# Kernel tuning notes

Hardware: AMD Instinct MI355X
Metric: run time of the kernel (lower is better)

The kernel has to match this reference:

```python
import jax, jax.numpy as jnp
import numpy as np

N_NODES = 20000
N_EDGES = 320000
H = 128
IN = 256  # num_hidden + num_in
SCALE = 30.0
EPS = 1e-5


def _ln(x, g, b):
    m = jnp.mean(x, axis=-1, keepdims=True)
    v = jnp.var(x, axis=-1, keepdims=True)
    return (x - m) * jax.lax.rsqrt(v + EPS) * g + b


def setup_inputs() -> dict:
    key = jax.random.key(0)
    ks = jax.random.split(key, 16)
    s_in = 1.0 / np.sqrt(IN)
    s_h = 1.0 / np.sqrt(H)
    s_4h = 1.0 / np.sqrt(4 * H)
    return {
        "h_V": jax.random.normal(ks[0], (N_NODES, H), jnp.float32),
        "h_E": jax.random.normal(ks[1], (N_EDGES, IN), jnp.float32),
        "edge_idx": jax.random.randint(ks[2], (2, N_EDGES), 0, N_NODES, jnp.int32),
        # weights stored (in, out): y = x @ W + b (equivalent to torch Linear)
        "W1_w": jax.random.uniform(ks[3], (IN, H), jnp.float32, -s_in, s_in),
        "W1_b": jax.random.uniform(ks[4], (H,), jnp.float32, -s_in, s_in),
        "W2_w": jax.random.uniform(ks[5], (H, H), jnp.float32, -s_h, s_h),
        "W2_b": jax.random.uniform(ks[6], (H,), jnp.float32, -s_h, s_h),
        "W3_w": jax.random.uniform(ks[7], (H, H), jnp.float32, -s_h, s_h),
        "W3_b": jax.random.uniform(ks[8], (H,), jnp.float32, -s_h, s_h),
        "n1_g": jnp.ones((H,), jnp.float32),
        "n1_b": jnp.zeros((H,), jnp.float32),
        "d1_w": jax.random.uniform(ks[9], (H, 4 * H), jnp.float32, -s_h, s_h),
        "d1_b": jax.random.uniform(ks[10], (4 * H,), jnp.float32, -s_h, s_h),
        "d2_w": jax.random.uniform(ks[11], (4 * H, H), jnp.float32, -s_4h, s_4h),
        "d2_b": jax.random.uniform(ks[12], (H,), jnp.float32, -s_4h, s_4h),
        "n2_g": jnp.ones((H,), jnp.float32),
        "n2_b": jnp.zeros((H,), jnp.float32),
    }


def reference(h_V, h_E, edge_idx, W1_w, W1_b, W2_w, W2_b, W3_w, W3_b,
              n1_g, n1_b, d1_w, d1_b, d2_w, d2_b, n2_g, n2_b):
    gelu = lambda x: jax.nn.gelu(x, approximate=False)  # torch F.gelu default = erf
    src_idx = edge_idx[0]
    # edge MLP: W3(gelu(W2(gelu(W1(h_E)))))
    h_message = gelu(h_E @ W1_w + W1_b)
    h_message = gelu(h_message @ W2_w + W2_b)
    h_message = h_message @ W3_w + W3_b
    # scatter_sum over source node, then scale
    dh = jax.ops.segment_sum(h_message, src_idx, num_segments=N_NODES) / SCALE
    h_V = _ln(h_V + dh, n1_g, n1_b)  # dropout is identity at eval
    dh = gelu(h_V @ d1_w + d1_b) @ d2_w + d2_b
    h_V = _ln(h_V + dh, n2_g, n2_b)
    return h_V
```

## Files before the change

### kernel.cpp

```cpp
#include <hip/hip_runtime.h>
#include <hip/hip_bf16.h>
#include <math.h>

#define NNODES 20000
#define NEDGES 320000
#define HDIM   128
#define INDIM  256
#define INV_SCALE (1.0f/30.0f)
#define LN_EPS 1e-5f

typedef __bf16 bf16x8 __attribute__((ext_vector_type(8)));
typedef float  f32x4  __attribute__((ext_vector_type(4)));
typedef _Float16 half4_t __attribute__((ext_vector_type(4)));
typedef _Float16 half8_t __attribute__((ext_vector_type(8)));
typedef unsigned short ushort_t;

__device__ __forceinline__ unsigned short f2bf(float f) {
    union { __hip_bfloat16 h; unsigned short u; } c;
    c.h = __float2bfloat16(f);
    return c.u;
}

__device__ __forceinline__ float gelu_fast(float x) {
    const float z = x * (1.595769122f + 0.071354816f * x * x);
    return x / (1.0f + __expf(-z));
}

__device__ __forceinline__ f32x4 mfma_bf16(bf16x8 a, bf16x8 b, f32x4 c) {
    return __builtin_amdgcn_mfma_f32_16x16x32_bf16(a, b, c, 0, 0, 0);
}

#define CVT8(dst, v0, v1) { union { bf16x8 v; ushort_t u[8]; } c_; \
    c_.u[0] = f2bf((v0).x); c_.u[1] = f2bf((v0).y); c_.u[2] = f2bf((v0).z); c_.u[3] = f2bf((v0).w); \
    c_.u[4] = f2bf((v1).x); c_.u[5] = f2bf((v1).y); c_.u[6] = f2bf((v1).z); c_.u[7] = f2bf((v1).w); \
    (dst) = c_.v; }

__global__ void prep_all(const float* __restrict__ W1, const float* __restrict__ W2,
                         const float* __restrict__ W3, ushort_t* __restrict__ WswE,
                         const float* __restrict__ D1, const float* __restrict__ D2,
                         ushort_t* __restrict__ D1sw, ushort_t* __restrict__ D2sw,
                         const int* __restrict__ src, int* __restrict__ cnt) {
    const int id = blockIdx.x * 256 + threadIdx.x;
    if (id < 65536) {
        const float* W; int base, idx; bool perm = false;
        if (id < 32768)      { W = W1; base = 0;     idx = id; }
        else if (id < 49152) { W = W2; base = 32768; idx = id - 32768; }
        else                 { W = W3; base = 49152; idx = id - 49152; perm = true; }
        const int j = idx & 7, lane = (idx >> 3) & 63, t = (idx >> 9) & 7, s = idx >> 12;
        const int k = s * 32 + (lane >> 4) * 8 + j;
        const int n = perm ? (2 * ((t >> 1) * 16 + (lane & 15)) + (t & 1))
                           : (t * 16 + (lane & 15));
        WswE[base + idx] = f2bf(W[k * HDIM + n]);
    } else if (id < 196608) {
        if (!D1sw) return;
        const int nid = id - 65536;
        if (nid < 65536) {
            const int idx = nid;
            const int j = idx & 7, lane = (idx >> 3) & 63, f = idx >> 9;
            const int t = f & 31, s = f >> 5;
            const int k = s * 32 + (lane >> 4) * 8 + j;
            const int n = t * 16 + (lane & 15);
            D1sw[idx] = f2bf(D1[k * 512 + n]);
        } else {
            const int idx = nid - 65536;
            const int j = idx & 7, lane = (idx >> 3) & 63, f = idx >> 9;
            const int t = f & 7, s = f >> 3;
            const int k = s * 32 + (lane >> 4) * 8 + j;
            const int n = t * 16 + (lane & 15);
            D2sw[idx] = f2bf(D2[k * HDIM + n]);
        }
    } else {
        if (!cnt) return;
        const int e = id - 196608;
        if (e < NEDGES) atomicAdd(&cnt[src[e]], 1);
    }
}

__launch_bounds__(1024)
__global__ void scan_counts(const int* __restrict__ cnt,
                            int* __restrict__ off, int* __restrict__ off2) {
    __shared__ int tot[1024];
    const int t = threadIdx.x;
    const int base = t * 20;
    int local[20]; int s = 0;
    #pragma unroll
    for (int i = 0; i < 20; ++i) {
        const int v = (base + i < NNODES) ? cnt[base + i] : 0;
        local[i] = s; s += v;
    }
    tot[t] = s;
    __syncthreads();
    for (int d = 1; d < 1024; d <<= 1) {
        const int v = (t >= d) ? tot[t - d] : 0;
        __syncthreads();
        tot[t] += v;
        __syncthreads();
    }
    const int excl = (t == 0) ? 0 : tot[t - 1];
    #pragma unroll
    for (int i = 0; i < 20; ++i)
        if (base + i < NNODES) { off[base + i] = excl + local[i]; off2[base + i] = excl + local[i]; }
    if (t == 1023) off[NNODES] = NEDGES;
}

__global__ void fill_perm(const int* __restrict__ src, int* __restrict__ off2,
                          int* __restrict__ perm) {
    const int e = blockIdx.x * 256 + threadIdx.x;
    if (e < NEDGES) {
        const int p = atomicAdd(&off2[src[e]], 1);
        perm[p] = e;
    }
}

#define A1H 136
#define SY  136

__launch_bounds__(256, 4)
__global__ void edge_mlp_v3(const float* __restrict__ hE,
                            const ushort_t* __restrict__ Wsw,
                            const float* __restrict__ b1,
                            const float* __restrict__ b2,
                            const float* __restrict__ b3,
                            _Float16* __restrict__ msg) {
    __shared__ __align__(16) ushort_t A1h[64 * A1H];
    __shared__ __align__(16) ushort_t A2[64 * SY];

    const int tid = threadIdx.x;
    const int wave = tid >> 6, lane = tid & 63;
    const int quad = lane >> 4, l16 = lane & 15;
    const size_t e0 = (size_t)blockIdx.x * 64;
    const int T0 = wave * 2;

    const int srow = tid >> 2, sq = tid & 3;
    const float4* sp = (const float4*)(hE + (e0 + srow) * INDIM) + sq * 8;
    ushort_t* sd = A1h + srow * A1H + sq * 32;

    float4 rg[8];
    #pragma unroll
    for (int i = 0; i < 8; ++i) rg[i] = sp[i];
    #pragma unroll
    for (int i = 0; i < 4; ++i) {
        bf16x8 v; CVT8(v, rg[2 * i], rg[2 * i + 1]);
        *(bf16x8*)(sd + i * 8) = v;
    }
    #pragma unroll
    for (int i = 0; i < 8; ++i) rg[i] = sp[32 + i];

    f32x4 acc[4][2];
    bf16x8 bcur[2], bnxt[2];

    #pragma unroll
    for (int t = 0; t < 2; ++t) {
        const float bv = b1[(T0 + t) * 16 + l16];
        #pragma unroll
        for (int rt = 0; rt < 4; ++rt) acc[rt][t] = (f32x4){bv, bv, bv, bv};
    }
    bcur[0] = *(const bf16x8*)(Wsw + (size_t)((T0 + 0) * 64 + lane) * 8);
    bcur[1] = *(const bf16x8*)(Wsw + (size_t)((T0 + 1) * 64 + lane) * 8);
    __syncthreads();

    #pragma unroll
    for (int s = 0; s < 4; ++s) {
        bnxt[0] = *(const bf16x8*)(Wsw + (size_t)(((s + 1) * 8 + T0 + 0) * 64 + lane) * 8);
        bnxt[1] = *(const bf16x8*)(Wsw + (size_t)(((s + 1) * 8 + T0 + 1) * 64 + lane) * 8);
        bf16x8 a[4];
        #pragma unroll
        for (int rt = 0; rt < 4; ++rt)
            a[rt] = *(const bf16x8*)(A1h + (rt * 16 + l16) * A1H + s * 32 + quad * 8);
        #pragma unroll
        for (int rt = 0; rt < 4; ++rt) {
            acc[rt][0] = mfma_bf16(a[rt], bcur[0], acc[rt][0]);
            acc[rt][1] = mfma_bf16(a[rt], bcur[1], acc[rt][1]);
        }
        bcur[0] = bnxt[0]; bcur[1] = bnxt[1];
    }
    __syncthreads();

    #pragma unroll
    for (int i = 0; i < 4; ++i) {
        bf16x8 v; CVT8(v, rg[2 * i], rg[2 * i + 1]);
        *(bf16x8*)(sd + i * 8) = v;
    }
    __syncthreads();

    #pragma unroll
    for (int s = 4; s < 8; ++s) {
        if (s < 7) {
            bnxt[0] = *(const bf16x8*)(Wsw + (size_t)(((s + 1) * 8 + T0 + 0) * 64 + lane) * 8);
            bnxt[1] = *(const bf16x8*)(Wsw + (size_t)(((s + 1) * 8 + T0 + 1) * 64 + lane) * 8);
        }
        bf16x8 a[4];
        #pragma unroll
        for (int rt = 0; rt < 4; ++rt)
            a[rt] = *(const bf16x8*)(A1h + (rt * 16 + l16) * A1H + (s - 4) * 32 + quad * 8);
        #pragma unroll
        for (int rt = 0; rt < 4; ++rt) {
            acc[rt][0] = mfma_bf16(a[rt], bcur[0], acc[rt][0]);
            acc[rt][1] = mfma_bf16(a[rt], bcur[1], acc[rt][1]);
        }
        bcur[0] = bnxt[0]; bcur[1] = bnxt[1];
    }
    #pragma unroll
    for (int rt = 0; rt < 4; ++rt)
        #pragma unroll
        for (int t = 0; t < 2; ++t)
            #pragma unroll
            for (int r = 0; r < 4; ++r)
                A2[(rt * 16 + quad * 4 + r) * SY + (T0 + t) * 16 + l16] =
                    f2bf(gelu_fast(acc[rt][t][r]));
    __syncthreads();

    #pragma unroll
    for (int t = 0; t < 2; ++t) {
        const float bv = b2[(T0 + t) * 16 + l16];
        #pragma unroll
        for (int rt = 0; rt < 4; ++rt) acc[rt][t] = (f32x4){bv, bv, bv, bv};
    }
    bcur[0] = *(const bf16x8*)(Wsw + 32768 + (size_t)((T0 + 0) * 64 + lane) * 8);
    bcur[1] = *(const bf16x8*)(Wsw + 32768 + (size_t)((T0 + 1) * 64 + lane) * 8);
    #pragma unroll
    for (int s = 0; s < 4; ++s) {
        if (s < 3) {
            bnxt[0] = *(const bf16x8*)(Wsw + 32768 + (size_t)(((s + 1) * 8 + T0 + 0) * 64 + lane) * 8);
            bnxt[1] = *(const bf16x8*)(Wsw + 32768 + (size_t)(((s + 1) * 8 + T0 + 1) * 64 + lane) * 8);
        }
        bf16x8 a[4];
        #pragma unroll
        for (int rt = 0; rt < 4; ++rt)
            a[rt] = *(const bf16x8*)(A2 + (rt * 16 + l16) * SY + s * 32 + quad * 8);
        #pragma unroll
        for (int rt = 0; rt < 4; ++rt) {
            acc[rt][0] = mfma_bf16(a[rt], bcur[0], acc[rt][0]);
            acc[rt][1] = mfma_bf16(a[rt], bcur[1], acc[rt][1]);
        }
        bcur[0] = bnxt[0]; bcur[1] = bnxt[1];
    }
    __syncthreads();
    #pragma unroll
    for (int rt = 0; rt < 4; ++rt)
        #pragma unroll
        for (int t = 0; t < 2; ++t)
            #pragma unroll
            for (int r = 0; r < 4; ++r)
                A2[(rt * 16 + quad * 4 + r) * SY + (T0 + t) * 16 + l16] =
                    f2bf(gelu_fast(acc[rt][t][r]));
    __syncthreads();

    #pragma unroll
    for (int t = 0; t < 2; ++t) {
        const float bv = b3[2 * (wave * 16 + l16) + t];
        #pragma unroll
        for (int rt = 0; rt < 4; ++rt) acc[rt][t] = (f32x4){bv, bv, bv, bv};
    }
    bcur[0] = *(const bf16x8*)(Wsw + 49152 + (size_t)((T0 + 0) * 64 + lane) * 8);
    bcur[1] = *(const bf16x8*)(Wsw + 49152 + (size_t)((T0 + 1) * 64 + lane) * 8);
    #pragma unroll
    for (int s = 0; s < 4; ++s) {
        if (s < 3) {
            bnxt[0] = *(const bf16x8*)(Wsw + 49152 + (size_t)(((s + 1) * 8 + T0 + 0) * 64 + lane) * 8);
            bnxt[1] = *(const bf16x8*)(Wsw + 49152 + (size_t)(((s + 1) * 8 + T0 + 1) * 64 + lane) * 8);
        }
        bf16x8 a[4];
        #pragma unroll
        for (int rt = 0; rt < 4; ++rt)
            a[rt] = *(const bf16x8*)(A2 + (rt * 16 + l16) * SY + s * 32 + quad * 8);
        #pragma unroll
        for (int rt = 0; rt < 4; ++rt) {
            acc[rt][0] = mfma_bf16(a[rt], bcur[0], acc[rt][0]);
            acc[rt][1] = mfma_bf16(a[rt], bcur[1], acc[rt][1]);
        }
        bcur[0] = bnxt[0]; bcur[1] = bnxt[1];
    }

    #pragma unroll
    for (int rt = 0; rt < 4; ++rt)
        #pragma unroll
        for (int r = 0; r < 4; ++r) {
            const size_t row = e0 + rt * 16 + quad * 4 + r;
            union { _Float16 h[2]; unsigned int u; } pk;
            pk.h[0] = (_Float16)acc[rt][0][r];
            pk.h[1] = (_Float16)acc[rt][1][r];
            ((unsigned int*)(msg + row * HDIM))[wave * 16 + l16] = pk.u;
        }
}

__launch_bounds__(256)
__global__ void gather_sum(const _Float16* __restrict__ msg,
                           const int* __restrict__ perm,
                           const int* __restrict__ off,
                           const float* __restrict__ hV,
                           float* __restrict__ xout) {
    const int tid = threadIdx.x;
    const int slot = tid >> 5, l32 = tid & 31;
    const int node = blockIdx.x * 8 + slot;
    const int j0 = off[node], j1 = off[node + 1];
    float a0 = 0.f, a1 = 0.f, a2 = 0.f, a3 = 0.f;
    int j = j0;
    for (; j + 1 < j1; j += 2) {
        const int ea = perm[j], eb = perm[j + 1];
        const half4_t ma = *(const half4_t*)(msg + (size_t)ea * HDIM + l32 * 4);
        const half4_t mb = *(const half4_t*)(msg + (size_t)eb * HDIM + l32 * 4);
        a0 += (float)ma[0] + (float)mb[0];
        a1 += (float)ma[1] + (float)mb[1];
        a2 += (float)ma[2] + (float)mb[2];
        a3 += (float)ma[3] + (float)mb[3];
    }
    if (j < j1) {
        const int ea = perm[j];
        const half4_t ma = *(const half4_t*)(msg + (size_t)ea * HDIM + l32 * 4);
        a0 += (float)ma[0]; a1 += (float)ma[1]; a2 += (float)ma[2]; a3 += (float)ma[3];
    }
    const float4 hv = *(const float4*)(hV + (size_t)node * HDIM + l32 * 4);
    const float4 o = {hv.x + a0 * INV_SCALE, hv.y + a1 * INV_SCALE,
                      hv.z + a2 * INV_SCALE, hv.w + a3 * INV_SCALE};
    *(float4*)(xout + (size_t)node * HDIM + l32 * 4) = o;
}

__launch_bounds__(256)
__global__ void node_mfma_x(const float* __restrict__ xin,
                            const float* __restrict__ n1g, const float* __restrict__ n1b,
                            const ushort_t* __restrict__ D1sw, const float* __restrict__ D1b,
                            const ushort_t* __restrict__ D2sw, const float* __restrict__ D2b,
                            const float* __restrict__ n2g, const float* __restrict__ n2b,
                            float* __restrict__ out) {
    __shared__ __align__(16) float xs[32 * HDIM];
    __shared__ __align__(16) ushort_t h1a[32 * SY];
    __shared__ __align__(16) ushort_t ua[32 * 520];
    __shared__ float mu_s[32], rs_s[32];

    const int tid = threadIdx.x;
    const int wave = tid >> 6, lane = tid & 63;
    const int quad = lane >> 4, l16 = lane & 15;
    const int n0 = blockIdx.x * 32;

    #pragma unroll
    for (int it = 0; it < 4; ++it) {
        const int f4 = it * 256 + tid;
        ((float4*)xs)[f4] = ((const float4*)(xin + (size_t)n0 * HDIM))[f4];
    }
    __syncthreads();

    {
        const int row = tid >> 3, q = tid & 7;
        float s = 0.f, s2 = 0.f;
        #pragma unroll
        for (int c = 0; c < 16; ++c) { const float v = xs[row * HDIM + q * 16 + c]; s += v; s2 += v * v; }
        #pragma unroll
        for (int o = 1; o < 8; o <<= 1) { s += __shfl_xor(s, o); s2 += __shfl_xor(s2, o); }
        if (q == 0) {
            const float m = s * (1.0f / HDIM);
            mu_s[row] = m;
            rs_s[row] = rsqrtf(s2 * (1.0f / HDIM) - m * m + LN_EPS);
        }
    }
    __syncthreads();

    #pragma unroll
    for (int it = 0; it < 2; ++it) {
        const int g = it * 256 + tid;
        const int row = g >> 4, col = (g & 15) * 8;
        const float mu = mu_s[row], rs = rs_s[row];
        union { bf16x8 v; ushort_t u[8]; } c;
        #pragma unroll
        for (int jj = 0; jj < 8; ++jj) {
            const float h1 = (xs[row * HDIM + col + jj] - mu) * rs * n1g[col + jj] + n1b[col + jj];
            c.u[jj] = f2bf(h1);
        }
        *(bf16x8*)(h1a + row * SY + col) = c.v;
    }
    __syncthreads();

    {
        f32x4 acc1[2][8];
        #pragma unroll
        for (int t = 0; t < 8; ++t) {
            const float bv = D1b[wave * 128 + t * 16 + l16];
            acc1[0][t] = (f32x4){bv, bv, bv, bv};
            acc1[1][t] = acc1[0][t];
        }
        #pragma unroll
        for (int s = 0; s < 4; ++s) {
            bf16x8 a[2];
            #pragma unroll
            for (int rt = 0; rt < 2; ++rt)
                a[rt] = *(const bf16x8*)(h1a + (rt * 16 + l16) * SY + s * 32 + quad * 8);
            #pragma unroll
            for (int t = 0; t < 8; ++t) {
                const bf16x8 b = *(const bf16x8*)(D1sw + (size_t)((s * 32 + wave * 8 + t) * 64 + lane) * 8);
                acc1[0][t] = mfma_bf16(a[0], b, acc1[0][t]);
                acc1[1][t] = mfma_bf16(a[1], b, acc1[1][t]);
            }
        }
        #pragma unroll
        for (int rt = 0; rt < 2; ++rt)
            #pragma unroll
            for (int t = 0; t < 8; ++t)
                #pragma unroll
                for (int r = 0; r < 4; ++r)
                    ua[(rt * 16 + quad * 4 + r) * 520 + wave * 128 + t * 16 + l16] =
                        f2bf(gelu_fast(acc1[rt][t][r]));
    }
    __syncthreads();

    f32x4 acc2[2][2];
    acc2[0][0] = (f32x4){0,0,0,0}; acc2[0][1] = acc2[0][0];
    acc2[1][0] = acc2[0][0];       acc2[1][1] = acc2[0][0];
    #pragma unroll
    for (int s = 0; s < 16; ++s) {
        bf16x8 a[2];
        #pragma unroll
        for (int rt = 0; rt < 2; ++rt)
            a[rt] = *(const bf16x8*)(ua + (rt * 16 + l16) * 520 + s * 32 + quad * 8);
        #pragma unroll
        for (int tt = 0; tt < 2; ++tt) {
            const bf16x8 b = *(const bf16x8*)(D2sw + (size_t)((s * 8 + wave * 2 + tt) * 64 + lane) * 8);
            acc2[0][tt] = mfma_bf16(a[0], b, acc2[0][tt]);
            acc2[1][tt] = mfma_bf16(a[1], b, acc2[1][tt]);
        }
    }
    __syncthreads();

    float* yf = (float*)ua;
    #pragma unroll
    for (int rt = 0; rt < 2; ++rt)
        #pragma unroll
        for (int tt = 0; tt < 2; ++tt)
            #pragma unroll
            for (int r = 0; r < 4; ++r) {
                const int row = rt * 16 + quad * 4 + r;
                const int col = wave * 32 + tt * 16 + l16;
                const float h1 = (xs[row * HDIM + col] - mu_s[row]) * rs_s[row] * n1g[col] + n1b[col];
                yf[row * HDIM + col] = h1 + acc2[rt][tt][r] + D2b[col];
            }
    __syncthreads();

    {
        const int row = tid >> 3, q = tid & 7;
        float s = 0.f, s2 = 0.f;
        #pragma unroll
        for (int c = 0; c < 16; ++c) { const float v = yf[row * HDIM + q * 16 + c]; s += v; s2 += v * v; }
        #pragma unroll
        for (int o = 1; o < 8; o <<= 1) { s += __shfl_xor(s, o); s2 += __shfl_xor(s2, o); }
        if (q == 0) {
            const float m = s * (1.0f / HDIM);
            mu_s[row] = m;
            rs_s[row] = rsqrtf(s2 * (1.0f / HDIM) - m * m + LN_EPS);
        }
    }
    __syncthreads();

    #pragma unroll
    for (int it = 0; it < 4; ++it) {
        const int f4 = it * 256 + tid;
        const int row = f4 >> 5, col = (f4 & 31) * 4;
        const float4 y = ((const float4*)yf)[f4];
        const float mu = mu_s[row], rs = rs_s[row];
        float4 o;
        o.x = (y.x - mu) * rs * n2g[col + 0] + n2b[col + 0];
        o.y = (y.y - mu) * rs * n2g[col + 1] + n2b[col + 1];
        o.z = (y.z - mu) * rs * n2g[col + 2] + n2b[col + 2];
        o.w = (y.w - mu) * rs * n2g[col + 3] + n2b[col + 3];
        ((float4*)(out + (size_t)n0 * HDIM))[f4] = o;
    }
}

__launch_bounds__(256, 4)
__global__ void edge_mlp_mfma(const float* __restrict__ hE,
                              const int* __restrict__ edge_idx,
                              const ushort_t* __restrict__ Wsw,
                              const float* __restrict__ b1,
                              const float* __restrict__ b2,
                              const float* __restrict__ b3,
                              _Float16* __restrict__ dh) {
    __shared__ ushort_t A2[4][32 * SY];

    const int tid = threadIdx.x;
    const int wave = tid >> 6, lane = tid & 63;
    const int quad = lane >> 4, l16 = lane & 15;
    const size_t e0 = (size_t)blockIdx.x * 128 + wave * 32;
    ushort_t* Aw = A2[wave];

    f32x4 acc[2][8];

    #pragma unroll
    for (int t = 0; t < 8; ++t) {
        const float bv = b1[t * 16 + l16];
        acc[0][t] = (f32x4){bv, bv, bv, bv};
        acc[1][t] = acc[0][t];
    }
    #pragma unroll
    for (int s = 0; s < 8; ++s) {
        bf16x8 a[2];
        #pragma unroll
        for (int rt = 0; rt < 2; ++rt) {
            const float4* p = (const float4*)(hE + (e0 + rt * 16 + l16) * INDIM + s * 32 + quad * 8);
            const float4 v0 = p[0], v1 = p[1];
            bf16x8 av; CVT8(av, v0, v1);
            a[rt] = av;
        }
        #pragma unroll
        for (int t = 0; t < 8; ++t) {
            const bf16x8 b = *(const bf16x8*)(Wsw + (size_t)((s * 8 + t) * 64 + lane) * 8);
            acc[0][t] = mfma_bf16(a[0], b, acc[0][t]);
            acc[1][t] = mfma_bf16(a[1], b, acc[1][t]);
        }
    }
    #pragma unroll
    for (int rt = 0; rt < 2; ++rt)
        #pragma unroll
        for (int t = 0; t < 8; ++t)
            #pragma unroll
            for (int r = 0; r < 4; ++r)
                Aw[(rt * 16 + quad * 4 + r) * SY + t * 16 + l16] = f2bf(gelu_fast(acc[rt][t][r]));

    #pragma unroll
    for (int t = 0; t < 8; ++t) {
        const float bv = b2[t * 16 + l16];
        acc[0][t] = (f32x4){bv, bv, bv, bv};
        acc[1][t] = acc[0][t];
    }
    #pragma unroll
    for (int s = 0; s < 4; ++s) {
        bf16x8 a[2];
        #pragma unroll
        for (int rt = 0; rt < 2; ++rt)
            a[rt] = *(const bf16x8*)(Aw + (rt * 16 + l16) * SY + s * 32 + quad * 8);
        #pragma unroll
        for (int t = 0; t < 8; ++t) {
            const bf16x8 b = *(const bf16x8*)(Wsw + 32768 + (size_t)((s * 8 + t) * 64 + lane) * 8);
            acc[0][t] = mfma_bf16(a[0], b, acc[0][t]);
            acc[1][t] = mfma_bf16(a[1], b, acc[1][t]);
        }
    }
    #pragma unroll
    for (int rt = 0; rt < 2; ++rt)
        #pragma unroll
        for (int t = 0; t < 8; ++t)
            #pragma unroll
            for (int r = 0; r < 4; ++r)
                Aw[(rt * 16 + quad * 4 + r) * SY + t * 16 + l16] = f2bf(gelu_fast(acc[rt][t][r]));

    #pragma unroll
    for (int t = 0; t < 8; ++t) {
        const float bv = b3[2 * ((t >> 1) * 16 + l16) + (t & 1)];
        acc[0][t] = (f32x4){bv, bv, bv, bv};
        acc[1][t] = acc[0][t];
    }
    #pragma unroll
    for (int s = 0; s < 4; ++s) {
        bf16x8 a[2];
        #pragma unroll
        for (int rt = 0; rt < 2; ++rt)
            a[rt] = *(const bf16x8*)(Aw + (rt * 16 + l16) * SY + s * 32 + quad * 8);
        #pragma unroll
        for (int t = 0; t < 8; ++t) {
            const bf16x8 b = *(const bf16x8*)(Wsw + 49152 + (size_t)((s * 8 + t) * 64 + lane) * 8);
            acc[0][t] = mfma_bf16(a[0], b, acc[0][t]);
            acc[1][t] = mfma_bf16(a[1], b, acc[1][t]);
        }
    }

    #pragma unroll
    for (int rt = 0; rt < 2; ++rt)
        #pragma unroll
        for (int r = 0; r < 4; ++r) {
            const int e = (int)e0 + rt * 16 + quad * 4 + r;
            const int s = edge_idx[e];
            _Float16* dst = dh + (size_t)s * HDIM;
            #pragma unroll
            for (int u = 0; u < 4; ++u) {
                const int c = 2 * (u * 16 + l16);
                union { _Float16 h[2]; unsigned int u32; } pk;
                pk.h[0] = (_Float16)acc[rt][2 * u][r];
                pk.h[1] = (_Float16)acc[rt][2 * u + 1][r];
                asm volatile("global_atomic_pk_add_f16 %0, %1, off"
                             :: "v"(dst + c), "v"(pk.u32) : "memory");
            }
        }
}

__launch_bounds__(256)
__global__ void node_mfma(const float* __restrict__ hV, const _Float16* __restrict__ dh,
                          const float* __restrict__ n1g, const float* __restrict__ n1b,
                          const ushort_t* __restrict__ D1sw, const float* __restrict__ D1b,
                          const ushort_t* __restrict__ D2sw, const float* __restrict__ D2b,
                          const float* __restrict__ n2g, const float* __restrict__ n2b,
                          float* __restrict__ out) {
    __shared__ __align__(16) float xs[32 * HDIM];
    __shared__ __align__(16) ushort_t h1a[32 * SY];
    __shared__ __align__(16) ushort_t ua[32 * 520];
    __shared__ float mu_s[32], rs_s[32];

    const int tid = threadIdx.x;
    const int wave = tid >> 6, lane = tid & 63;
    const int quad = lane >> 4, l16 = lane & 15;
    const int n0 = blockIdx.x * 32;

    #pragma unroll
    for (int it = 0; it < 4; ++it) {
        const int f4 = it * 256 + tid;
        const float4 hv = ((const float4*)(hV + (size_t)n0 * HDIM))[f4];
        const half4_t dv = ((const half4_t*)(dh + (size_t)n0 * HDIM))[f4];
        ((float4*)xs)[f4] = (float4){hv.x + (float)dv[0] * INV_SCALE,
                                     hv.y + (float)dv[1] * INV_SCALE,
                                     hv.z + (float)dv[2] * INV_SCALE,
                                     hv.w + (float)dv[3] * INV_SCALE};
    }
    __syncthreads();

    {
        const int row = tid >> 3, q = tid & 7;
        float s = 0.f, s2 = 0.f;
        #pragma unroll
        for (int c = 0; c < 16; ++c) { const float v = xs[row * HDIM + q * 16 + c]; s += v; s2 += v * v; }
        #pragma unroll
        for (int o = 1; o < 8; o <<= 1) { s += __shfl_xor(s, o); s2 += __shfl_xor(s2, o); }
        if (q == 0) {
            const float m = s * (1.0f / HDIM);
            mu_s[row] = m;
            rs_s[row] = rsqrtf(s2 * (1.0f / HDIM) - m * m + LN_EPS);
        }
    }
    __syncthreads();

    #pragma unroll
    for (int it = 0; it < 2; ++it) {
        const int g = it * 256 + tid;
        const int row = g >> 4, col = (g & 15) * 8;
        const float mu = mu_s[row], rs = rs_s[row];
        union { bf16x8 v; ushort_t u[8]; } c;
        #pragma unroll
        for (int jj = 0; jj < 8; ++jj) {
            const float h1 = (xs[row * HDIM + col + jj] - mu) * rs * n1g[col + jj] + n1b[col + jj];
            c.u[jj] = f2bf(h1);
        }
        *(bf16x8*)(h1a + row * SY + col) = c.v;
    }
    __syncthreads();

    {
        f32x4 acc1[2][8];
        #pragma unroll
        for (int t = 0; t < 8; ++t) {
            const float bv = D1b[wave * 128 + t * 16 + l16];
            acc1[0][t] = (f32x4){bv, bv, bv, bv};
            acc1[1][t] = acc1[0][t];
        }
        #pragma unroll
        for (int s = 0; s < 4; ++s) {
            bf16x8 a[2];
            #pragma unroll
            for (int rt = 0; rt < 2; ++rt)
                a[rt] = *(const bf16x8*)(h1a + (rt * 16 + l16) * SY + s * 32 + quad * 8);
            #pragma unroll
            for (int t = 0; t < 8; ++t) {
                const bf16x8 b = *(const bf16x8*)(D1sw + (size_t)((s * 32 + wave * 8 + t) * 64 + lane) * 8);
                acc1[0][t] = mfma_bf16(a[0], b, acc1[0][t]);
                acc1[1][t] = mfma_bf16(a[1], b, acc1[1][t]);
            }
        }
        #pragma unroll
        for (int rt = 0; rt < 2; ++rt)
            #pragma unroll
            for (int t = 0; t < 8; ++t)
                #pragma unroll
                for (int r = 0; r < 4; ++r)
                    ua[(rt * 16 + quad * 4 + r) * 520 + wave * 128 + t * 16 + l16] =
                        f2bf(gelu_fast(acc1[rt][t][r]));
    }
    __syncthreads();

    f32x4 acc2[2][2];
    acc2[0][0] = (f32x4){0,0,0,0}; acc2[0][1] = acc2[0][0];
    acc2[1][0] = acc2[0][0];       acc2[1][1] = acc2[0][0];
    #pragma unroll
    for (int s = 0; s < 16; ++s) {
        bf16x8 a[2];
        #pragma unroll
        for (int rt = 0; rt < 2; ++rt)
            a[rt] = *(const bf16x8*)(ua + (rt * 16 + l16) * 520 + s * 32 + quad * 8);
        #pragma unroll
        for (int tt = 0; tt < 2; ++tt) {
            const bf16x8 b = *(const bf16x8*)(D2sw + (size_t)((s * 8 + wave * 2 + tt) * 64 + lane) * 8);
            acc2[0][tt] = mfma_bf16(a[0], b, acc2[0][tt]);
            acc2[1][tt] = mfma_bf16(a[1], b, acc2[1][tt]);
        }
    }
    __syncthreads();

    float* yf = (float*)ua;
    #pragma unroll
    for (int rt = 0; rt < 2; ++rt)
        #pragma unroll
        for (int tt = 0; tt < 2; ++tt)
            #pragma unroll
            for (int r = 0; r < 4; ++r) {
                const int row = rt * 16 + quad * 4 + r;
                const int col = wave * 32 + tt * 16 + l16;
                const float h1 = (xs[row * HDIM + col] - mu_s[row]) * rs_s[row] * n1g[col] + n1b[col];
                yf[row * HDIM + col] = h1 + acc2[rt][tt][r] + D2b[col];
            }
    __syncthreads();

    {
        const int row = tid >> 3, q = tid & 7;
        float s = 0.f, s2 = 0.f;
        #pragma unroll
        for (int c = 0; c < 16; ++c) { const float v = yf[row * HDIM + q * 16 + c]; s += v; s2 += v * v; }
        #pragma unroll
        for (int o = 1; o < 8; o <<= 1) { s += __shfl_xor(s, o); s2 += __shfl_xor(s2, o); }
        if (q == 0) {
            const float m = s * (1.0f / HDIM);
            mu_s[row] = m;
            rs_s[row] = rsqrtf(s2 * (1.0f / HDIM) - m * m + LN_EPS);
        }
    }
    __syncthreads();

    #pragma unroll
    for (int it = 0; it < 4; ++it) {
        const int f4 = it * 256 + tid;
        const int row = f4 >> 5, col = (f4 & 31) * 4;
        const float4 y = ((const float4*)yf)[f4];
        const float mu = mu_s[row], rs = rs_s[row];
        float4 o;
        o.x = (y.x - mu) * rs * n2g[col + 0] + n2b[col + 0];
        o.y = (y.y - mu) * rs * n2g[col + 1] + n2b[col + 1];
        o.z = (y.z - mu) * rs * n2g[col + 2] + n2b[col + 2];
        o.w = (y.w - mu) * rs * n2g[col + 3] + n2b[col + 3];
        ((float4*)(out + (size_t)n0 * HDIM))[f4] = o;
    }
}

#define NT 8
__device__ __forceinline__ void ln_stats32(const float* __restrict__ buf,
                                           float* __restrict__ mu_s,
                                           float* __restrict__ rs_s, int tid) {
    const int g = tid >> 5, lane = tid & 31;
    float s = 0.f, s2 = 0.f;
    #pragma unroll
    for (int c = lane; c < HDIM; c += 32) { const float v = buf[g * HDIM + c]; s += v; s2 += v * v; }
    #pragma unroll
    for (int o = 16; o; o >>= 1) { s += __shfl_xor(s, o, 32); s2 += __shfl_xor(s2, o, 32); }
    if (lane == 0) {
        const float m = s * (1.0f / HDIM);
        mu_s[g] = m;
        rs_s[g] = rsqrtf(s2 * (1.0f / HDIM) - m * m + LN_EPS);
    }
}

__launch_bounds__(256)
__global__ void node_update_f32(const float* __restrict__ hV, const _Float16* __restrict__ dh,
                                const float* __restrict__ n1g, const float* __restrict__ n1b,
                                const float* __restrict__ D1w, const float* __restrict__ D1b,
                                const float* __restrict__ D2w, const float* __restrict__ D2b,
                                const float* __restrict__ n2g, const float* __restrict__ n2b,
                                float* __restrict__ out) {
    __shared__ float h1s[NT * HDIM];
    __shared__ float us[NT * 512];
    __shared__ float vs[2 * NT * HDIM];
    __shared__ float mu_s[NT], rs_s[NT];
    const int tid = threadIdx.x;
    const int n0 = blockIdx.x * NT;
    for (int idx = tid; idx < NT * HDIM; idx += 256) {
        const int i = idx >> 7, c = idx & 127;
        const size_t g = (size_t)(n0 + i) * HDIM + c;
        h1s[idx] = hV[g] + (float)dh[g] * INV_SCALE;
    }
    __syncthreads();
    ln_stats32(h1s, mu_s, rs_s, tid);
    __syncthreads();
    for (int idx = tid; idx < NT * HDIM; idx += 256) {
        const int i = idx >> 7, c = idx & 127;
        h1s[idx] = (h1s[idx] - mu_s[i]) * rs_s[i] * n1g[c] + n1b[c];
    }
    __syncthreads();
    {
        const int o = 2 * tid;
        const float2 bv = *(const float2*)(D1b + o);
        float a0[NT], a1[NT];
        #pragma unroll
        for (int i = 0; i < NT; ++i) { a0[i] = bv.x; a1[i] = bv.y; }
        for (int k = 0; k < HDIM; ++k) {
            const float2 w = *(const float2*)(D1w + (size_t)k * 512 + o);
            #pragma unroll
            for (int i = 0; i < NT; ++i) {
                const float xv = h1s[i * HDIM + k];
                a0[i] += xv * w.x; a1[i] += xv * w.y;
            }
        }
        #pragma unroll
        for (int i = 0; i < NT; ++i) {
            us[i * 512 + o]     = gelu_fast(a0[i]);
            us[i * 512 + o + 1] = gelu_fast(a1[i]);
        }
    }
    __syncthreads();
    {
        const int o = tid & 127, half = tid >> 7;
        float a[NT];
        #pragma unroll
        for (int i = 0; i < NT; ++i) a[i] = 0.f;
        const int k0 = half * 256;
        for (int k = k0; k < k0 + 256; ++k) {
            const float w = D2w[(size_t)k * HDIM + o];
            #pragma unroll
            for (int i = 0; i < NT; ++i) a[i] += us[i * 512 + k] * w;
        }
        #pragma unroll
        for (int i = 0; i < NT; ++i) vs[(half * NT + i) * HDIM + o] = a[i];
    }
    __syncthreads();
    float* ys = us;
    for (int idx = tid; idx < NT * HDIM; idx += 256) {
        const int i = idx >> 7, c = idx & 127;
        ys[idx] = h1s[idx] + vs[i * HDIM + c] + vs[(NT + i) * HDIM + c] + D2b[c];
    }
    __syncthreads();
    ln_stats32(ys, mu_s, rs_s, tid);
    __syncthreads();
    for (int idx = tid; idx < NT * HDIM; idx += 256) {
        const int i = idx >> 7, c = idx & 127;
        out[(size_t)(n0 + i) * HDIM + c] = (ys[idx] - mu_s[i]) * rs_s[i] * n2g[c] + n2b[c];
    }
}

extern "C" void kernel_launch(void* const* d_in, const int* in_sizes, int n_in,
                              void* d_out, int out_size, void* d_ws, size_t ws_size,
                              hipStream_t stream) {
    const float* hV  = (const float*)d_in[0];
    const float* hE  = (const float*)d_in[1];
    const int*  eidx = (const int*)d_in[2];
    const float* W1w = (const float*)d_in[3];
    const float* W1b = (const float*)d_in[4];
    const float* W2w = (const float*)d_in[5];
    const float* W2b = (const float*)d_in[6];
    const float* W3w = (const float*)d_in[7];
    const float* W3b = (const float*)d_in[8];
    const float* n1g = (const float*)d_in[9];
    const float* n1b = (const float*)d_in[10];
    const float* D1w = (const float*)d_in[11];
    const float* D1b = (const float*)d_in[12];
    const float* D2w = (const float*)d_in[13];
    const float* D2b = (const float*)d_in[14];
    const float* n2g = (const float*)d_in[15];
    const float* n2b = (const float*)d_in[16];
    float* out = (float*)d_out;

    const size_t MSG_BYTES = (size_t)NEDGES * HDIM * sizeof(_Float16);
    const size_t EW_BYTES  = 65536 * 2;
    const size_t T1_BYTES  = MSG_BYTES + 3 * EW_BYTES
                           + (size_t)NEDGES * 4 + (size_t)NNODES * 4
                           + (size_t)(NNODES + 1) * 4 + (size_t)NNODES * 4;
    const size_t DH_BYTES  = (size_t)NNODES * HDIM * sizeof(_Float16);
    const size_t T2_BYTES  = DH_BYTES + 3 * EW_BYTES;

    if (ws_size >= T1_BYTES) {
        char* p = (char*)d_ws;
        _Float16* msg  = (_Float16*)p;            p += MSG_BYTES;
        ushort_t* WswE = (ushort_t*)p;            p += EW_BYTES;
        ushort_t* D1sw = (ushort_t*)p;            p += EW_BYTES;
        ushort_t* D2sw = (ushort_t*)p;            p += EW_BYTES;
        int* perm = (int*)p;                      p += (size_t)NEDGES * 4;
        int* cnt  = (int*)p;                      p += (size_t)NNODES * 4;
        int* off  = (int*)p;                      p += (size_t)(NNODES + 1) * 4;
        int* off2 = (int*)p;

        hipMemsetAsync(cnt, 0, (size_t)NNODES * 4, stream);
        prep_all<<<2019, 256, 0, stream>>>(W1w, W2w, W3w, WswE, D1w, D2w, D1sw, D2sw, eidx, cnt);
        scan_counts<<<1, 1024, 0, stream>>>(cnt, off, off2);
        fill_perm<<<(NEDGES + 255) / 256, 256, 0, stream>>>(eidx, off2, perm);
        edge_mlp_v3<<<NEDGES / 64, 256, 0, stream>>>(hE, WswE, W1b, W2b, W3b, msg);
        gather_sum<<<NNODES / 8, 256, 0, stream>>>(msg, perm, off, hV, out);
        node_mfma_x<<<NNODES / 32, 256, 0, stream>>>(out, n1g, n1b,
                                                     D1sw, D1b, D2sw, D2b, n2g, n2b, out);
    } else if (ws_size >= T2_BYTES) {
        _Float16* dh = (_Float16*)d_ws;
        ushort_t* WswE = (ushort_t*)((char*)d_ws + DH_BYTES);
        ushort_t* D1sw = (ushort_t*)((char*)d_ws + DH_BYTES + EW_BYTES);
        ushort_t* D2sw = (ushort_t*)((char*)d_ws + DH_BYTES + 2 * EW_BYTES);
        hipMemsetAsync(dh, 0, DH_BYTES, stream);
        prep_all<<<2019, 256, 0, stream>>>(W1w, W2w, W3w, WswE, D1w, D2w, D1sw, D2sw,
                                           eidx, nullptr);
        edge_mlp_mfma<<<NEDGES / 128, 256, 0, stream>>>(hE, eidx, WswE, W1b, W2b, W3b, dh);
        node_mfma<<<NNODES / 32, 256, 0, stream>>>(hV, dh, n1g, n1b, D1sw, D1b, D2sw, D2b, n2g, n2b, out);
    } else {
        _Float16* dh = (_Float16*)d_ws;
        ushort_t* WswE = (ushort_t*)((char*)d_out + (size_t)out_size * 4 - EW_BYTES);
        hipMemsetAsync(dh, 0, DH_BYTES, stream);
        prep_all<<<2019, 256, 0, stream>>>(W1w, W2w, W3w, WswE, D1w, D2w, nullptr, nullptr,
                                           eidx, nullptr);
        edge_mlp_mfma<<<NEDGES / 128, 256, 0, stream>>>(hE, eidx, WswE, W1b, W2b, W3b, dh);
        node_update_f32<<<NNODES / NT, 256, 0, stream>>>(hV, dh, n1g, n1b, D1w, D1b, D2w, D2b, n2g, n2b, out);
    }
}
```

Baseline: 615.4 us.

## Replace CSR gather path with atomic fp16 scatter fused into edge MLP

Removes the counting, scan, permutation and gather kernels and the full per-edge fp16 message buffer. The v3 edge MLP now scatters its output straight into a per-node fp16 accumulator using packed fp16 global atomics. The node kernel then reads that accumulator as before. This saves a large intermediate write/read and several launches, in exchange for atomic contention and fp16 accumulation precision in the sum.

```diff
diff --git a/kernel.cpp b/kernel.cpp
--- a/kernel.cpp
+++ b/kernel.cpp
@@ -12,7 +12,6 @@
 typedef __bf16 bf16x8 __attribute__((ext_vector_type(8)));
 typedef float  f32x4  __attribute__((ext_vector_type(4)));
 typedef _Float16 half4_t __attribute__((ext_vector_type(4)));
-typedef _Float16 half8_t __attribute__((ext_vector_type(8)));
 typedef unsigned short ushort_t;
 
 __device__ __forceinline__ unsigned short f2bf(float f) {
@@ -35,11 +34,10 @@
     c_.u[4] = f2bf((v1).x); c_.u[5] = f2bf((v1).y); c_.u[6] = f2bf((v1).z); c_.u[7] = f2bf((v1).w); \
     (dst) = c_.v; }
 
-__global__ void prep_all(const float* __restrict__ W1, const float* __restrict__ W2,
-                         const float* __restrict__ W3, ushort_t* __restrict__ WswE,
-                         const float* __restrict__ D1, const float* __restrict__ D2,
-                         ushort_t* __restrict__ D1sw, ushort_t* __restrict__ D2sw,
-                         const int* __restrict__ src, int* __restrict__ cnt) {
+__global__ void prep_weights(const float* __restrict__ W1, const float* __restrict__ W2,
+                             const float* __restrict__ W3, ushort_t* __restrict__ WswE,
+                             const float* __restrict__ D1, const float* __restrict__ D2,
+                             ushort_t* __restrict__ D1sw, ushort_t* __restrict__ D2sw) {
     const int id = blockIdx.x * 256 + threadIdx.x;
     if (id < 65536) {
         const float* W; int base, idx; bool perm = false;
@@ -51,7 +49,7 @@
         const int n = perm ? (2 * ((t >> 1) * 16 + (lane & 15)) + (t & 1))
                            : (t * 16 + (lane & 15));
         WswE[base + idx] = f2bf(W[k * HDIM + n]);
-    } else if (id < 196608) {
+    } else {
         if (!D1sw) return;
         const int nid = id - 65536;
         if (nid < 65536) {
@@ -69,46 +67,6 @@
             const int n = t * 16 + (lane & 15);
             D2sw[idx] = f2bf(D2[k * HDIM + n]);
         }
-    } else {
-        if (!cnt) return;
-        const int e = id - 196608;
-        if (e < NEDGES) atomicAdd(&cnt[src[e]], 1);
-    }
-}
-
-__launch_bounds__(1024)
-__global__ void scan_counts(const int* __restrict__ cnt,
-                            int* __restrict__ off, int* __restrict__ off2) {
-    __shared__ int tot[1024];
-    const int t = threadIdx.x;
-    const int base = t * 20;
-    int local[20]; int s = 0;
-    #pragma unroll
-    for (int i = 0; i < 20; ++i) {
-        const int v = (base + i < NNODES) ? cnt[base + i] : 0;
-        local[i] = s; s += v;
-    }
-    tot[t] = s;
-    __syncthreads();
-    for (int d = 1; d < 1024; d <<= 1) {
-        const int v = (t >= d) ? tot[t - d] : 0;
-        __syncthreads();
-        tot[t] += v;
-        __syncthreads();
-    }
-    const int excl = (t == 0) ? 0 : tot[t - 1];
-    #pragma unroll
-    for (int i = 0; i < 20; ++i)
-        if (base + i < NNODES) { off[base + i] = excl + local[i]; off2[base + i] = excl + local[i]; }
-    if (t == 1023) off[NNODES] = NEDGES;
-}
-
-__global__ void fill_perm(const int* __restrict__ src, int* __restrict__ off2,
-                          int* __restrict__ perm) {
-    const int e = blockIdx.x * 256 + threadIdx.x;
-    if (e < NEDGES) {
-        const int p = atomicAdd(&off2[src[e]], 1);
-        perm[p] = e;
     }
 }
 
@@ -116,12 +74,13 @@
 #define SY  136
 
 __launch_bounds__(256, 4)
-__global__ void edge_mlp_v3(const float* __restrict__ hE,
+__global__ void edge_mlp_v4(const float* __restrict__ hE,
+                            const int* __restrict__ edge_idx,
                             const ushort_t* __restrict__ Wsw,
                             const float* __restrict__ b1,
                             const float* __restrict__ b2,
                             const float* __restrict__ b3,
-                            _Float16* __restrict__ msg) {
+                            _Float16* __restrict__ dh) {
     __shared__ __align__(16) ushort_t A1h[64 * A1H];
     __shared__ __align__(16) ushort_t A2[64 * SY];
 
@@ -272,310 +231,19 @@
         bcur[0] = bnxt[0]; bcur[1] = bnxt[1];
     }
 
+    const int ccol = 2 * (wave * 16 + l16);
     #pragma unroll
     for (int rt = 0; rt < 4; ++rt)
         #pragma unroll
         for (int r = 0; r < 4; ++r) {
-            const size_t row = e0 + rt * 16 + quad * 4 + r;
+            const int row = (int)e0 + rt * 16 + quad * 4 + r;
+            const int s = edge_idx[row];
+            _Float16* dst = dh + (size_t)s * HDIM + ccol;
             union { _Float16 h[2]; unsigned int u; } pk;
             pk.h[0] = (_Float16)acc[rt][0][r];
             pk.h[1] = (_Float16)acc[rt][1][r];
-            ((unsigned int*)(msg + row * HDIM))[wave * 16 + l16] = pk.u;
-        }
-}
-
-__launch_bounds__(256)
-__global__ void gather_sum(const _Float16* __restrict__ msg,
-                           const int* __restrict__ perm,
-                           const int* __restrict__ off,
-                           const float* __restrict__ hV,
-                           float* __restrict__ xout) {
-    const int tid = threadIdx.x;
-    const int slot = tid >> 5, l32 = tid & 31;
-    const int node = blockIdx.x * 8 + slot;
-    const int j0 = off[node], j1 = off[node + 1];
-    float a0 = 0.f, a1 = 0.f, a2 = 0.f, a3 = 0.f;
-    int j = j0;
-    for (; j + 1 < j1; j += 2) {
-        const int ea = perm[j], eb = perm[j + 1];
-        const half4_t ma = *(const half4_t*)(msg + (size_t)ea * HDIM + l32 * 4);
-        const half4_t mb = *(const half4_t*)(msg + (size_t)eb * HDIM + l32 * 4);
-        a0 += (float)ma[0] + (float)mb[0];
-        a1 += (float)ma[1] + (float)mb[1];
-        a2 += (float)ma[2] + (float)mb[2];
-        a3 += (float)ma[3] + (float)mb[3];
-    }
-    if (j < j1) {
-        const int ea = perm[j];
-        const half4_t ma = *(const half4_t*)(msg + (size_t)ea * HDIM + l32 * 4);
-        a0 += (float)ma[0]; a1 += (float)ma[1]; a2 += (float)ma[2]; a3 += (float)ma[3];
-    }
-    const float4 hv = *(const float4*)(hV + (size_t)node * HDIM + l32 * 4);
-    const float4 o = {hv.x + a0 * INV_SCALE, hv.y + a1 * INV_SCALE,
-                      hv.z + a2 * INV_SCALE, hv.w + a3 * INV_SCALE};
-    *(float4*)(xout + (size_t)node * HDIM + l32 * 4) = o;
-}
-
-__launch_bounds__(256)
-__global__ void node_mfma_x(const float* __restrict__ xin,
-                            const float* __restrict__ n1g, const float* __restrict__ n1b,
-                            const ushort_t* __restrict__ D1sw, const float* __restrict__ D1b,
-                            const ushort_t* __restrict__ D2sw, const float* __restrict__ D2b,
-                            const float* __restrict__ n2g, const float* __restrict__ n2b,
-                            float* __restrict__ out) {
-    __shared__ __align__(16) float xs[32 * HDIM];
-    __shared__ __align__(16) ushort_t h1a[32 * SY];
-    __shared__ __align__(16) ushort_t ua[32 * 520];
-    __shared__ float mu_s[32], rs_s[32];
-
-    const int tid = threadIdx.x;
-    const int wave = tid >> 6, lane = tid & 63;
-    const int quad = lane >> 4, l16 = lane & 15;
-    const int n0 = blockIdx.x * 32;
-
-    #pragma unroll
-    for (int it = 0; it < 4; ++it) {
-        const int f4 = it * 256 + tid;
-        ((float4*)xs)[f4] = ((const float4*)(xin + (size_t)n0 * HDIM))[f4];
-    }
-    __syncthreads();
-
-    {
-        const int row = tid >> 3, q = tid & 7;
-        float s = 0.f, s2 = 0.f;
-        #pragma unroll
-        for (int c = 0; c < 16; ++c) { const float v = xs[row * HDIM + q * 16 + c]; s += v; s2 += v * v; }
-        #pragma unroll
-        for (int o = 1; o < 8; o <<= 1) { s += __shfl_xor(s, o); s2 += __shfl_xor(s2, o); }
-        if (q == 0) {
-            const float m = s * (1.0f / HDIM);
-            mu_s[row] = m;
-            rs_s[row] = rsqrtf(s2 * (1.0f / HDIM) - m * m + LN_EPS);
-        }
-    }
-    __syncthreads();
-
-    #pragma unroll
-    for (int it = 0; it < 2; ++it) {
-        const int g = it * 256 + tid;
-        const int row = g >> 4, col = (g & 15) * 8;
-        const float mu = mu_s[row], rs = rs_s[row];
-        union { bf16x8 v; ushort_t u[8]; } c;
-        #pragma unroll
-        for (int jj = 0; jj < 8; ++jj) {
-            const float h1 = (xs[row * HDIM + col + jj] - mu) * rs * n1g[col + jj] + n1b[col + jj];
-            c.u[jj] = f2bf(h1);
-        }
-        *(bf16x8*)(h1a + row * SY + col) = c.v;
-    }
-    __syncthreads();
-
-    {
-        f32x4 acc1[2][8];
-        #pragma unroll
-        for (int t = 0; t < 8; ++t) {
-            const float bv = D1b[wave * 128 + t * 16 + l16];
-            acc1[0][t] = (f32x4){bv, bv, bv, bv};
-            acc1[1][t] = acc1[0][t];
-        }
-        #pragma unroll
-        for (int s = 0; s < 4; ++s) {
-            bf16x8 a[2];
-            #pragma unroll
-            for (int rt = 0; rt < 2; ++rt)
-                a[rt] = *(const bf16x8*)(h1a + (rt * 16 + l16) * SY + s * 32 + quad * 8);
-            #pragma unroll
-            for (int t = 0; t < 8; ++t) {
-                const bf16x8 b = *(const bf16x8*)(D1sw + (size_t)((s * 32 + wave * 8 + t) * 64 + lane) * 8);
-                acc1[0][t] = mfma_bf16(a[0], b, acc1[0][t]);
-                acc1[1][t] = mfma_bf16(a[1], b, acc1[1][t]);
-            }
-        }
-        #pragma unroll
-        for (int rt = 0; rt < 2; ++rt)
-            #pragma unroll
-            for (int t = 0; t < 8; ++t)
-                #pragma unroll
-                for (int r = 0; r < 4; ++r)
-                    ua[(rt * 16 + quad * 4 + r) * 520 + wave * 128 + t * 16 + l16] =
-                        f2bf(gelu_fast(acc1[rt][t][r]));
-    }
-    __syncthreads();
-
-    f32x4 acc2[2][2];
-    acc2[0][0] = (f32x4){0,0,0,0}; acc2[0][1] = acc2[0][0];
-    acc2[1][0] = acc2[0][0];       acc2[1][1] = acc2[0][0];
-    #pragma unroll
-    for (int s = 0; s < 16; ++s) {
-        bf16x8 a[2];
-        #pragma unroll
-        for (int rt = 0; rt < 2; ++rt)
-            a[rt] = *(const bf16x8*)(ua + (rt * 16 + l16) * 520 + s * 32 + quad * 8);
-        #pragma unroll
-        for (int tt = 0; tt < 2; ++tt) {
-            const bf16x8 b = *(const bf16x8*)(D2sw + (size_t)((s * 8 + wave * 2 + tt) * 64 + lane) * 8);
-            acc2[0][tt] = mfma_bf16(a[0], b, acc2[0][tt]);
-            acc2[1][tt] = mfma_bf16(a[1], b, acc2[1][tt]);
-        }
-    }
-    __syncthreads();
-
-    float* yf = (float*)ua;
-    #pragma unroll
-    for (int rt = 0; rt < 2; ++rt)
-        #pragma unroll
-        for (int tt = 0; tt < 2; ++tt)
-            #pragma unroll
-            for (int r = 0; r < 4; ++r) {
-                const int row = rt * 16 + quad * 4 + r;
-                const int col = wave * 32 + tt * 16 + l16;
-                const float h1 = (xs[row * HDIM + col] - mu_s[row]) * rs_s[row] * n1g[col] + n1b[col];
-                yf[row * HDIM + col] = h1 + acc2[rt][tt][r] + D2b[col];
-            }
-    __syncthreads();
-
-    {
-        const int row = tid >> 3, q = tid & 7;
-        float s = 0.f, s2 = 0.f;
-        #pragma unroll
-        for (int c = 0; c < 16; ++c) { const float v = yf[row * HDIM + q * 16 + c]; s += v; s2 += v * v; }
-        #pragma unroll
-        for (int o = 1; o < 8; o <<= 1) { s += __shfl_xor(s, o); s2 += __shfl_xor(s2, o); }
-        if (q == 0) {
-            const float m = s * (1.0f / HDIM);
-            mu_s[row] = m;
-            rs_s[row] = rsqrtf(s2 * (1.0f / HDIM) - m * m + LN_EPS);
-        }
-    }
-    __syncthreads();
-
-    #pragma unroll
-    for (int it = 0; it < 4; ++it) {
-        const int f4 = it * 256 + tid;
-        const int row = f4 >> 5, col = (f4 & 31) * 4;
-        const float4 y = ((const float4*)yf)[f4];
-        const float mu = mu_s[row], rs = rs_s[row];
-        float4 o;
-        o.x = (y.x - mu) * rs * n2g[col + 0] + n2b[col + 0];
-        o.y = (y.y - mu) * rs * n2g[col + 1] + n2b[col + 1];
-        o.z = (y.z - mu) * rs * n2g[col + 2] + n2b[col + 2];
-        o.w = (y.w - mu) * rs * n2g[col + 3] + n2b[col + 3];
-        ((float4*)(out + (size_t)n0 * HDIM))[f4] = o;
-    }
-}
-
-__launch_bounds__(256, 4)
-__global__ void edge_mlp_mfma(const float* __restrict__ hE,
-                              const int* __restrict__ edge_idx,
-                              const ushort_t* __restrict__ Wsw,
-                              const float* __restrict__ b1,
-                              const float* __restrict__ b2,
-                              const float* __restrict__ b3,
-                              _Float16* __restrict__ dh) {
-    __shared__ ushort_t A2[4][32 * SY];
-
-    const int tid = threadIdx.x;
-    const int wave = tid >> 6, lane = tid & 63;
-    const int quad = lane >> 4, l16 = lane & 15;
-    const size_t e0 = (size_t)blockIdx.x * 128 + wave * 32;
-    ushort_t* Aw = A2[wave];
-
-    f32x4 acc[2][8];
-
-    #pragma unroll
-    for (int t = 0; t < 8; ++t) {
-        const float bv = b1[t * 16 + l16];
-        acc[0][t] = (f32x4){bv, bv, bv, bv};
-        acc[1][t] = acc[0][t];
-    }
-    #pragma unroll
-    for (int s = 0; s < 8; ++s) {
-        bf16x8 a[2];
-        #pragma unroll
-        for (int rt = 0; rt < 2; ++rt) {
-            const float4* p = (const float4*)(hE + (e0 + rt * 16 + l16) * INDIM + s * 32 + quad * 8);
-            const float4 v0 = p[0], v1 = p[1];
-            bf16x8 av; CVT8(av, v0, v1);
-            a[rt] = av;
-        }
-        #pragma unroll
-        for (int t = 0; t < 8; ++t) {
-            const bf16x8 b = *(const bf16x8*)(Wsw + (size_t)((s * 8 + t) * 64 + lane) * 8);
-            acc[0][t] = mfma_bf16(a[0], b, acc[0][t]);
-            acc[1][t] = mfma_bf16(a[1], b, acc[1][t]);
-        }
-    }
-    #pragma unroll
-    for (int rt = 0; rt < 2; ++rt)
-        #pragma unroll
-        for (int t = 0; t < 8; ++t)
-            #pragma unroll
-            for (int r = 0; r < 4; ++r)
-                Aw[(rt * 16 + quad * 4 + r) * SY + t * 16 + l16] = f2bf(gelu_fast(acc[rt][t][r]));
-
-    #pragma unroll
-    for (int t = 0; t < 8; ++t) {
-        const float bv = b2[t * 16 + l16];
-        acc[0][t] = (f32x4){bv, bv, bv, bv};
-        acc[1][t] = acc[0][t];
-    }
-    #pragma unroll
-    for (int s = 0; s < 4; ++s) {
-        bf16x8 a[2];
-        #pragma unroll
-        for (int rt = 0; rt < 2; ++rt)
-            a[rt] = *(const bf16x8*)(Aw + (rt * 16 + l16) * SY + s * 32 + quad * 8);
-        #pragma unroll
-        for (int t = 0; t < 8; ++t) {
-            const bf16x8 b = *(const bf16x8*)(Wsw + 32768 + (size_t)((s * 8 + t) * 64 + lane) * 8);
-            acc[0][t] = mfma_bf16(a[0], b, acc[0][t]);
-            acc[1][t] = mfma_bf16(a[1], b, acc[1][t]);
-        }
-    }
-    #pragma unroll
-    for (int rt = 0; rt < 2; ++rt)
-        #pragma unroll
-        for (int t = 0; t < 8; ++t)
-            #pragma unroll
-            for (int r = 0; r < 4; ++r)
-                Aw[(rt * 16 + quad * 4 + r) * SY + t * 16 + l16] = f2bf(gelu_fast(acc[rt][t][r]));
-
-    #pragma unroll
-    for (int t = 0; t < 8; ++t) {
-        const float bv = b3[2 * ((t >> 1) * 16 + l16) + (t & 1)];
-        acc[0][t] = (f32x4){bv, bv, bv, bv};
-        acc[1][t] = acc[0][t];
-    }
-    #pragma unroll
-    for (int s = 0; s < 4; ++s) {
-        bf16x8 a[2];
-        #pragma unroll
-        for (int rt = 0; rt < 2; ++rt)
-            a[rt] = *(const bf16x8*)(Aw + (rt * 16 + l16) * SY + s * 32 + quad * 8);
-        #pragma unroll
-        for (int t = 0; t < 8; ++t) {
-            const bf16x8 b = *(const bf16x8*)(Wsw + 49152 + (size_t)((s * 8 + t) * 64 + lane) * 8);
-            acc[0][t] = mfma_bf16(a[0], b, acc[0][t]);
-            acc[1][t] = mfma_bf16(a[1], b, acc[1][t]);
-        }
-    }
-
-    #pragma unroll
-    for (int rt = 0; rt < 2; ++rt)
-        #pragma unroll
-        for (int r = 0; r < 4; ++r) {
-            const int e = (int)e0 + rt * 16 + quad * 4 + r;
-            const int s = edge_idx[e];
-            _Float16* dst = dh + (size_t)s * HDIM;
-            #pragma unroll
-            for (int u = 0; u < 4; ++u) {
-                const int c = 2 * (u * 16 + l16);
-                union { _Float16 h[2]; unsigned int u32; } pk;
-                pk.h[0] = (_Float16)acc[rt][2 * u][r];
-                pk.h[1] = (_Float16)acc[rt][2 * u + 1][r];
-                asm volatile("global_atomic_pk_add_f16 %0, %1, off"
-                             :: "v"(dst + c), "v"(pk.u32) : "memory");
-            }
+            asm volatile("global_atomic_pk_add_f16 %0, %1, off"
+                         :: "v"(dst), "v"(pk.u) : "memory");
         }
 }
 
@@ -847,50 +515,24 @@
     const float* n2b = (const float*)d_in[16];
     float* out = (float*)d_out;
 
-    const size_t MSG_BYTES = (size_t)NEDGES * HDIM * sizeof(_Float16);
-    const size_t EW_BYTES  = 65536 * 2;
-    const size_t T1_BYTES  = MSG_BYTES + 3 * EW_BYTES
-                           + (size_t)NEDGES * 4 + (size_t)NNODES * 4
-                           + (size_t)(NNODES + 1) * 4 + (size_t)NNODES * 4;
-    const size_t DH_BYTES  = (size_t)NNODES * HDIM * sizeof(_Float16);
-    const size_t T2_BYTES  = DH_BYTES + 3 * EW_BYTES;
-
-    if (ws_size >= T1_BYTES) {
-        char* p = (char*)d_ws;
-        _Float16* msg  = (_Float16*)p;            p += MSG_BYTES;
-        ushort_t* WswE = (ushort_t*)p;            p += EW_BYTES;
-        ushort_t* D1sw = (ushort_t*)p;            p += EW_BYTES;
-        ushort_t* D2sw = (ushort_t*)p;            p += EW_BYTES;
-        int* perm = (int*)p;                      p += (size_t)NEDGES * 4;
-        int* cnt  = (int*)p;                      p += (size_t)NNODES * 4;
-        int* off  = (int*)p;                      p += (size_t)(NNODES + 1) * 4;
-        int* off2 = (int*)p;
-
-        hipMemsetAsync(cnt, 0, (size_t)NNODES * 4, stream);
-        prep_all<<<2019, 256, 0, stream>>>(W1w, W2w, W3w, WswE, D1w, D2w, D1sw, D2sw, eidx, cnt);
-        scan_counts<<<1, 1024, 0, stream>>>(cnt, off, off2);
-        fill_perm<<<(NEDGES + 255) / 256, 256, 0, stream>>>(eidx, off2, perm);
-        edge_mlp_v3<<<NEDGES / 64, 256, 0, stream>>>(hE, WswE, W1b, W2b, W3b, msg);
-        gather_sum<<<NNODES / 8, 256, 0, stream>>>(msg, perm, off, hV, out);
-        node_mfma_x<<<NNODES / 32, 256, 0, stream>>>(out, n1g, n1b,
-                                                     D1sw, D1b, D2sw, D2b, n2g, n2b, out);
-    } else if (ws_size >= T2_BYTES) {
-        _Float16* dh = (_Float16*)d_ws;
+    const size_t DH_BYTES = (size_t)NNODES * HDIM * sizeof(_Float16);
+    const size_t EW_BYTES = 65536 * 2;
+    const size_t T_MAIN   = DH_BYTES + 3 * EW_BYTES;
+
+    _Float16* dh = (_Float16*)d_ws;
+    hipMemsetAsync(dh, 0, DH_BYTES, stream);
+
+    if (ws_size >= T_MAIN) {
         ushort_t* WswE = (ushort_t*)((char*)d_ws + DH_BYTES);
         ushort_t* D1sw = (ushort_t*)((char*)d_ws + DH_BYTES + EW_BYTES);
         ushort_t* D2sw = (ushort_t*)((char*)d_ws + DH_BYTES + 2 * EW_BYTES);
-        hipMemsetAsync(dh, 0, DH_BYTES, stream);
-        prep_all<<<2019, 256, 0, stream>>>(W1w, W2w, W3w, WswE, D1w, D2w, D1sw, D2sw,
-                                           eidx, nullptr);
-        edge_mlp_mfma<<<NEDGES / 128, 256, 0, stream>>>(hE, eidx, WswE, W1b, W2b, W3b, dh);
+        prep_weights<<<768, 256, 0, stream>>>(W1w, W2w, W3w, WswE, D1w, D2w, D1sw, D2sw);
+        edge_mlp_v4<<<NEDGES / 64, 256, 0, stream>>>(hE, eidx, WswE, W1b, W2b, W3b, dh);
         node_mfma<<<NNODES / 32, 256, 0, stream>>>(hV, dh, n1g, n1b, D1sw, D1b, D2sw, D2b, n2g, n2b, out);
     } else {
-        _Float16* dh = (_Float16*)d_ws;
         ushort_t* WswE = (ushort_t*)((char*)d_out + (size_t)out_size * 4 - EW_BYTES);
-        hipMemsetAsync(dh, 0, DH_BYTES, stream);
-        prep_all<<<2019, 256, 0, stream>>>(W1w, W2w, W3w, WswE, D1w, D2w, nullptr, nullptr,
-                                           eidx, nullptr);
-        edge_mlp_mfma<<<NEDGES / 128, 256, 0, stream>>>(hE, eidx, WswE, W1b, W2b, W3b, dh);
+        prep_weights<<<256, 256, 0, stream>>>(W1w, W2w, W3w, WswE, D1w, D2w, nullptr, nullptr);
+        edge_mlp_v4<<<NEDGES / 64, 256, 0, stream>>>(hE, eidx, WswE, W1b, W2b, W3b, dh);
         node_update_f32<<<NNODES / NT, 256, 0, stream>>>(hV, dh, n1g, n1b, D1w, D1b, D2w, D2b, n2g, n2b, out);
     }
 }
```

Result: faster. 553.1 us (-10.1%).
